# Optimization experiments

Measured on AMD Instinct MI355X. Metric: run time of the kernel, lower is better.

Reference implementation:

```python
import jax, jax.numpy as jnp
from jax import lax
import numpy as np

VOCAB, EMB, SEQ, HID, BATCH = 50000, 300, 80, 128, 4096


def setup_inputs() -> dict:
    key = jax.random.key(0)
    ks = jax.random.split(key, 7)
    x = jax.random.randint(ks[0], (BATCH, SEQ), 0, VOCAB)
    emb = jax.random.normal(ks[1], (VOCAB, EMB), jnp.float32) * 0.05  # frozen pretrained table
    # Keras SimpleRNN: kernel (glorot), recurrent_kernel (orthogonal-ish), bias zeros
    Wxh = jax.random.normal(ks[2], (EMB, HID), jnp.float32) * (1.0 / np.sqrt(EMB))
    Whh = jax.random.normal(ks[3], (HID, HID), jnp.float32) * (1.0 / np.sqrt(HID))
    bh = jnp.zeros((HID,), jnp.float32)
    Wd = jax.random.normal(ks[4], (HID, 1), jnp.float32) * (1.0 / np.sqrt(HID))
    bd = jnp.zeros((1,), jnp.float32)
    return {"x": x, "emb": emb, "Wxh": Wxh, "Whh": Whh, "bh": bh, "Wd": Wd, "bd": bd}


def reference(x, emb, Wxh, Whh, bh, Wd, bd):
    # Embedding lookup: [B, T] -> [B, T, E]
    e = emb[x]
    # Precompute input projection for all timesteps: [B, T, H]
    xp = jnp.einsum('bte,eh->bth', e, Wxh) + bh
    # SimpleRNN recurrence (tanh), return only last hidden state
    def step(h, xt):  # xt: [B, H]
        h = jnp.tanh(xt + h @ Whh)
        return h, None
    h0 = jnp.zeros((x.shape[0], Whh.shape[0]), xp.dtype)
    h_last, _ = lax.scan(step, h0, jnp.swapaxes(xp, 0, 1))  # scan over time
    # Dense(1, sigmoid): [B, 1]
    return jax.nn.sigmoid(h_last @ Wd + bd)
```

## Files before the change

kernel.cpp:

```cpp
#include <hip/hip_runtime.h>
#include <hip/hip_fp16.h>
#include <cstdint>

#define VOCAB 50000
#define EMB   300
#define SEQ   80
#define HID   128
#define BATCH 4096

typedef __attribute__((ext_vector_type(8))) _Float16 f16x8;
typedef __attribute__((ext_vector_type(4))) float    f32x4;

static __device__ __forceinline__ float fast_tanh(float xv) {
    const float e = __expf(2.f * xv);
    float r;
    asm("v_rcp_f32 %0, %1" : "=v"(r) : "v"(e + 1.f));
    return fmaf(-2.f, r, 1.f);
}
static __device__ __forceinline__ float f16b2f(unsigned short u) {
    _Float16 h; __builtin_memcpy(&h, &u, 2); return (float)h;
}
static __device__ __forceinline__ unsigned pack2h(float a, float b) {
    _Float16 ha = (_Float16)a, hb = (_Float16)b;
    unsigned short ua, ub;
    __builtin_memcpy(&ua, &ha, 2); __builtin_memcpy(&ub, &hb, 2);
    return (unsigned)ua | ((unsigned)ub << 16);
}

__global__ __launch_bounds__(256) void k_wprep(const float* __restrict__ Wxh,
                                               _Float16* __restrict__ W2) {
    const int c = blockIdx.x * 256 + threadIdx.x;
    if (c >= 5120) return;
    const int ks = c >> 9, rem = c & 511, col = rem >> 2, g = rem & 3;
    f16x8 f;
    #pragma unroll
    for (int j = 0; j < 8; ++j) {
        const int k = 32 * ks + 8 * g + j;
        f[j] = (_Float16)(k < EMB ? Wxh[k * HID + col] : 0.f);
    }
    *reinterpret_cast<f16x8*>(W2 + (size_t)c * 8) = f;
}

__global__ __launch_bounds__(256, 2) void k_ptab(
    const float*    __restrict__ emb,
    const _Float16* __restrict__ W2,
    const float*    __restrict__ bh,
    float*          __restrict__ P)
{
    const int tid = threadIdx.x, lane = tid & 63;
    const int wv = tid >> 6, r16 = lane & 15, g = lane >> 4;
    const int row = blockIdx.x * 64 + wv * 16 + r16;
    const float* rp = emb + (size_t)(row < VOCAB ? row : VOCAB - 1) * EMB;
    const bool wr = (row < VOCAB);

    f16x8 ef[10];
    #pragma unroll
    for (int ks = 0; ks < 9; ++ks) {
        const float4 u0 = *reinterpret_cast<const float4*>(rp + 32 * ks + 8 * g);
        const float4 u1 = *reinterpret_cast<const float4*>(rp + 32 * ks + 8 * g + 4);
        f16x8 f;
        f[0] = (_Float16)u0.x; f[1] = (_Float16)u0.y;
        f[2] = (_Float16)u0.z; f[3] = (_Float16)u0.w;
        f[4] = (_Float16)u1.x; f[5] = (_Float16)u1.y;
        f[6] = (_Float16)u1.z; f[7] = (_Float16)u1.w;
        ef[ks] = f;
    }
    {
        f16x8 f;
        #pragma unroll
        for (int j = 0; j < 8; ++j) f[j] = (_Float16)0.f;
        if (g == 0) {
            const float4 u0 = *reinterpret_cast<const float4*>(rp + 288);
            const float4 u1 = *reinterpret_cast<const float4*>(rp + 292);
            f[0] = (_Float16)u0.x; f[1] = (_Float16)u0.y;
            f[2] = (_Float16)u0.z; f[3] = (_Float16)u0.w;
            f[4] = (_Float16)u1.x; f[5] = (_Float16)u1.y;
            f[6] = (_Float16)u1.z; f[7] = (_Float16)u1.w;
        } else if (g == 1) {
            const float4 u0 = *reinterpret_cast<const float4*>(rp + 296);
            f[0] = (_Float16)u0.x; f[1] = (_Float16)u0.y;
            f[2] = (_Float16)u0.z; f[3] = (_Float16)u0.w;
        }
        ef[9] = f;
    }

    float4 bhf[8];
    #pragma unroll
    for (int ct = 0; ct < 8; ++ct)
        bhf[ct] = *reinterpret_cast<const float4*>(bh + 16 * ct + 4 * g);

    f16x8 wA[10], wB[10];
    #pragma unroll
    for (int ks = 0; ks < 10; ++ks)
        wA[ks] = *reinterpret_cast<const f16x8*>(
            W2 + ((size_t)ks * 512 + (size_t)r16 * 4 + g) * 8);

    float* const po = P + (size_t)(wr ? row : 0) * HID;

    #pragma unroll
    for (int ct = 0; ct < 8; ++ct) {
        if (ct < 7) {
            const int coln = 16 * (ct + 1) + r16;
            #pragma unroll
            for (int ks = 0; ks < 10; ++ks)
                ((ct & 1) ? wA : wB)[ks] = *reinterpret_cast<const f16x8*>(
                    W2 + ((size_t)ks * 512 + (size_t)coln * 4 + g) * 8);
        }
        const f16x8* wc = (ct & 1) ? wB : wA;
        f32x4 a0 = {0.f, 0.f, 0.f, 0.f}, a1 = {0.f, 0.f, 0.f, 0.f};
        #pragma unroll
        for (int ks = 0; ks < 10; ks += 2) {
            a0 = __builtin_amdgcn_mfma_f32_16x16x32_f16(wc[ks],     ef[ks],     a0, 0, 0, 0);
            a1 = __builtin_amdgcn_mfma_f32_16x16x32_f16(wc[ks + 1], ef[ks + 1], a1, 0, 0, 0);
        }
        float4 o;
        o.x = a0[0] + a1[0] + bhf[ct].x;
        o.y = a0[1] + a1[1] + bhf[ct].y;
        o.z = a0[2] + a1[2] + bhf[ct].z;
        o.w = a0[3] + a1[3] + bhf[ct].w;
        if (wr) *reinterpret_cast<float4*>(po + ct * 16 + g * 4) = o;
    }
}

__global__ __launch_bounds__(512, 2) void k_rnn(
    const int*   __restrict__ x,
    const float* __restrict__ P,
    const float* __restrict__ Whh,
    const float* __restrict__ Wd,
    const float* __restrict__ bd,
    float*       __restrict__ out)
{
    __shared__ __align__(16) unsigned char Hb[2][16 * 256];

    const int tid = threadIdx.x, lane = tid & 63, wv = tid >> 6;
    const int r16 = lane & 15, g = lane >> 4;
    const int rb = blockIdx.x * 16;
    const int xbase = (rb + r16) * SEQ;

    if (tid < 256) { uint4 z = {}; *reinterpret_cast<uint4*>(&Hb[0][tid * 16]) = z; }

    const int col = 16 * wv + r16;

    int h_rd[4];
    #pragma unroll
    for (int ks = 0; ks < 4; ++ks)
        h_rd[ks] = r16 * 256 + (((4 * ks + g) ^ r16) & 15) * 16;
    const int hw = r16 * 256 + (((2 * wv + (g >> 1)) ^ r16) & 15) * 16 + (g & 1) * 8;

    f16x8 wh[4];
    #pragma unroll
    for (int ks = 0; ks < 4; ++ks) {
        f16x8 f;
        #pragma unroll
        for (int j = 0; j < 8; ++j)
            f[j] = (_Float16)Whh[(32 * ks + 8 * g + j) * HID + col];
        wh[ks] = f;
    }

    const int goff = 16 * wv + 4 * g;
    f32x4 xgA, xgB;
    int idxA, idxB;
    {
        const int i0 = x[xbase + 0];
        const int i1 = x[xbase + 1];
        xgA = *reinterpret_cast<const f32x4*>(P + (size_t)i0 * HID + goff);
        xgB = *reinterpret_cast<const f32x4*>(P + (size_t)i1 * HID + goff);
        idxA = x[xbase + 2];
        idxB = x[xbase + 3];
    }

    __syncthreads();

    const f32x4 z4 = {0.f, 0.f, 0.f, 0.f};
    f32x4 accA, accB;

#define STEP(T, PB, XG, IDX)                                                       \
    {                                                                              \
        const unsigned char* hb = &Hb[PB][0];                                      \
        const f16x8 h0 = *reinterpret_cast<const f16x8*>(hb + h_rd[0]);            \
        const f16x8 h1 = *reinterpret_cast<const f16x8*>(hb + h_rd[1]);            \
        const f16x8 h2 = *reinterpret_cast<const f16x8*>(hb + h_rd[2]);            \
        const f16x8 h3 = *reinterpret_cast<const f16x8*>(hb + h_rd[3]);            \
        accA = __builtin_amdgcn_mfma_f32_16x16x32_f16(wh[0], h0, XG, 0, 0, 0);     \
        accB = __builtin_amdgcn_mfma_f32_16x16x32_f16(wh[1], h1, z4, 0, 0, 0);     \
        accA = __builtin_amdgcn_mfma_f32_16x16x32_f16(wh[2], h2, accA, 0, 0, 0);   \
        accB = __builtin_amdgcn_mfma_f32_16x16x32_f16(wh[3], h3, accB, 0, 0, 0);   \
                  \
        if ((T) + 2 < SEQ) {                                                       \
            XG = *reinterpret_cast<const f32x4*>(P + (size_t)(IDX) * HID + goff);  \
            if ((T) + 4 < SEQ) IDX = x[xbase + (T) + 4];                           \
        }                                                                          \
        uint2 hv;                                                                  \
        hv.x = pack2h(fast_tanh(accA[0] + accB[0]), fast_tanh(accA[1] + accB[1])); \
        hv.y = pack2h(fast_tanh(accA[2] + accB[2]), fast_tanh(accA[3] + accB[3])); \
        *reinterpret_cast<uint2*>(&Hb[(PB) ^ 1][hw]) = hv;                         \
        asm volatile("s_waitcnt lgkmcnt(0)" ::: "memory");                         \
        __builtin_amdgcn_s_barrier();                                              \
        __builtin_amdgcn_sched_barrier(0);                                         \
    }

    #pragma unroll 1
    for (int t = 0; t < SEQ; t += 2) {
        STEP(t,     0, xgA, idxA);
        STEP(t + 1, 1, xgB, idxB);
    }
#undef STEP

    const char* hb0 = (const char*)&Hb[0][0];
    const int r = tid >> 5, m = tid & 31;
    const int fb = r * 256 + (((m >> 1) ^ r) & 15) * 16 + (m & 1) * 8;
    const uint2 hv = *reinterpret_cast<const uint2*>(hb0 + fb);
    const float4 wd = *reinterpret_cast<const float4*>(&Wd[4 * m]);
    float part = f16b2f((unsigned short)(hv.x & 0xffff)) * wd.x
               + f16b2f((unsigned short)(hv.x >> 16))    * wd.y
               + f16b2f((unsigned short)(hv.y & 0xffff)) * wd.z
               + f16b2f((unsigned short)(hv.y >> 16))    * wd.w;
    part += __shfl_down(part, 16, 32);
    part += __shfl_down(part, 8, 32);
    part += __shfl_down(part, 4, 32);
    part += __shfl_down(part, 2, 32);
    part += __shfl_down(part, 1, 32);
    if (m == 0) out[rb + r] = 1.f / (1.f + expf(-(part + bd[0])));
}

extern "C" void kernel_launch(void* const* d_in, const int* in_sizes, int n_in,
                              void* d_out, int out_size, void* d_ws, size_t ws_size,
                              hipStream_t stream)
{
    (void)in_sizes; (void)n_in; (void)out_size; (void)ws_size;
    const int*   x   = (const int*)  d_in[0];
    const float* emb = (const float*)d_in[1];
    const float* Wxh = (const float*)d_in[2];
    const float* Whh = (const float*)d_in[3];
    const float* bh  = (const float*)d_in[4];
    const float* Wd  = (const float*)d_in[5];
    const float* bd  = (const float*)d_in[6];
    float* out = (float*)d_out;

    float*    P  = (float*)d_ws;
    _Float16* W2 = (_Float16*)((char*)d_ws + 25600000);

    k_wprep<<<20, 256, 0, stream>>>(Wxh, W2);
    k_ptab<<<(VOCAB + 63) / 64, 256, 0, stream>>>(emb, W2, bh, P);
    k_rnn<<<BATCH / 16, 512, 0, stream>>>(x, P, Whh, Wd, bd, out);
}
```

Before: 81.65 us.

## Store projection table in fp16 and stage per-step gathers through LDS

The precomputed vocab projection table P is now written in fp16, which halves its size and the write/read traffic in both kernels. In the RNN kernel the token indices for the block are preloaded into LDS. Half the threads gather full 256-byte P rows as coalesced 16-byte loads into a double-buffered LDS tile one step ahead, and each wave reads its slice from LDS as the MFMA accumulator init. This costs extra LDS traffic per step and a small fp16 rounding of the input projection, and the step loop is no longer held to unroll 1.

```diff
diff --git a/kernel.cpp b/kernel.cpp
--- a/kernel.cpp
+++ b/kernel.cpp
@@ -45,7 +45,7 @@
     const float*    __restrict__ emb,
     const _Float16* __restrict__ W2,
     const float*    __restrict__ bh,
-    float*          __restrict__ P)
+    _Float16*       __restrict__ P)
 {
     const int tid = threadIdx.x, lane = tid & 63;
     const int wv = tid >> 6, r16 = lane & 15, g = lane >> 4;
@@ -95,7 +95,7 @@
         wA[ks] = *reinterpret_cast<const f16x8*>(
             W2 + ((size_t)ks * 512 + (size_t)r16 * 4 + g) * 8);
 
-    float* const po = P + (size_t)(wr ? row : 0) * HID;
+    unsigned short* const po = (unsigned short*)P + (size_t)(wr ? row : 0) * HID;
 
     #pragma unroll
     for (int ct = 0; ct < 8; ++ct) {
@@ -113,30 +113,30 @@
             a0 = __builtin_amdgcn_mfma_f32_16x16x32_f16(wc[ks],     ef[ks],     a0, 0, 0, 0);
             a1 = __builtin_amdgcn_mfma_f32_16x16x32_f16(wc[ks + 1], ef[ks + 1], a1, 0, 0, 0);
         }
-        float4 o;
-        o.x = a0[0] + a1[0] + bhf[ct].x;
-        o.y = a0[1] + a1[1] + bhf[ct].y;
-        o.z = a0[2] + a1[2] + bhf[ct].z;
-        o.w = a0[3] + a1[3] + bhf[ct].w;
-        if (wr) *reinterpret_cast<float4*>(po + ct * 16 + g * 4) = o;
+        uint2 o;
+        o.x = pack2h(a0[0] + a1[0] + bhf[ct].x, a0[1] + a1[1] + bhf[ct].y);
+        o.y = pack2h(a0[2] + a1[2] + bhf[ct].z, a0[3] + a1[3] + bhf[ct].w);
+        if (wr) *reinterpret_cast<uint2*>(po + ct * 16 + g * 4) = o;
     }
 }
 
 __global__ __launch_bounds__(512, 2) void k_rnn(
-    const int*   __restrict__ x,
-    const float* __restrict__ P,
-    const float* __restrict__ Whh,
-    const float* __restrict__ Wd,
-    const float* __restrict__ bd,
-    float*       __restrict__ out)
+    const int*      __restrict__ x,
+    const _Float16* __restrict__ P,
+    const float*    __restrict__ Whh,
+    const float*    __restrict__ Wd,
+    const float*    __restrict__ bd,
+    float*          __restrict__ out)
 {
+    __shared__ __align__(16) unsigned char Xb[2][16 * 256];
     __shared__ __align__(16) unsigned char Hb[2][16 * 256];
+    __shared__ int xidx[16 * SEQ];
 
     const int tid = threadIdx.x, lane = tid & 63, wv = tid >> 6;
     const int r16 = lane & 15, g = lane >> 4;
     const int rb = blockIdx.x * 16;
-    const int xbase = (rb + r16) * SEQ;
-
+
+    for (int q = tid; q < 16 * SEQ; q += 512) xidx[q] = x[rb * SEQ + q];
     if (tid < 256) { uint4 z = {}; *reinterpret_cast<uint4*>(&Hb[0][tid * 16]) = z; }
 
     const int col = 16 * wv + r16;
@@ -157,39 +157,44 @@
         wh[ks] = f;
     }
 
-    const int goff = 16 * wv + 4 * g;
-    f32x4 xgA, xgB;
-    int idxA, idxB;
-    {
-        const int i0 = x[xbase + 0];
-        const int i1 = x[xbase + 1];
-        xgA = *reinterpret_cast<const f32x4*>(P + (size_t)i0 * HID + goff);
-        xgB = *reinterpret_cast<const f32x4*>(P + (size_t)i1 * HID + goff);
-        idxA = x[xbase + 2];
-        idxB = x[xbase + 3];
-    }
+    const bool gon  = (tid < 256);
+    const int  grow = (tid >> 4) & 15, gk = tid & 15;
+    const int  gdst = grow * 256 + ((gk ^ grow) & 15) * 16;
 
     __syncthreads();
 
-    const f32x4 z4 = {0.f, 0.f, 0.f, 0.f};
-    f32x4 accA, accB;
-
-#define STEP(T, PB, XG, IDX)                                                       \
+    if (gon)
+        *reinterpret_cast<uint4*>(&Xb[0][gdst]) = *reinterpret_cast<const uint4*>(
+            P + (size_t)xidx[grow * SEQ] * HID + 8 * gk);
+    uint4 cur = {}, nxt = {};
+    if (gon) cur = *reinterpret_cast<const uint4*>(
+        P + (size_t)xidx[grow * SEQ + 1] * HID + 8 * gk);
+
+    asm volatile("s_waitcnt lgkmcnt(0)" ::: "memory");
+    __builtin_amdgcn_s_barrier();
+    __builtin_amdgcn_sched_barrier(0);
+
+#define STEP(T, PB, CUR, NXT)                                                      \
     {                                                                              \
-        const unsigned char* hb = &Hb[PB][0];                                      \
-        const f16x8 h0 = *reinterpret_cast<const f16x8*>(hb + h_rd[0]);            \
-        const f16x8 h1 = *reinterpret_cast<const f16x8*>(hb + h_rd[1]);            \
-        const f16x8 h2 = *reinterpret_cast<const f16x8*>(hb + h_rd[2]);            \
-        const f16x8 h3 = *reinterpret_cast<const f16x8*>(hb + h_rd[3]);            \
-        accA = __builtin_amdgcn_mfma_f32_16x16x32_f16(wh[0], h0, XG, 0, 0, 0);     \
-        accB = __builtin_amdgcn_mfma_f32_16x16x32_f16(wh[1], h1, z4, 0, 0, 0);     \
+        if ((T) + 1 < SEQ && gon)                                                  \
+            *reinterpret_cast<uint4*>(&Xb[(PB) ^ 1][gdst]) = CUR;                  \
+        if ((T) + 2 < SEQ && gon)                                                  \
+            NXT = *reinterpret_cast<const uint4*>(                                 \
+                P + (size_t)xidx[grow * SEQ + (T) + 2] * HID + 8 * gk);            \
+        const uint2 xv = *reinterpret_cast<const uint2*>(&Xb[PB][hw]);             \
+        f32x4 accA, accB = {0.f, 0.f, 0.f, 0.f};                                   \
+        accA[0] = f16b2f((unsigned short)(xv.x & 0xffff));                         \
+        accA[1] = f16b2f((unsigned short)(xv.x >> 16));                            \
+        accA[2] = f16b2f((unsigned short)(xv.y & 0xffff));                         \
+        accA[3] = f16b2f((unsigned short)(xv.y >> 16));                            \
+        const f16x8 h0 = *reinterpret_cast<const f16x8*>(&Hb[PB][h_rd[0]]);        \
+        const f16x8 h1 = *reinterpret_cast<const f16x8*>(&Hb[PB][h_rd[1]]);        \
+        const f16x8 h2 = *reinterpret_cast<const f16x8*>(&Hb[PB][h_rd[2]]);        \
+        const f16x8 h3 = *reinterpret_cast<const f16x8*>(&Hb[PB][h_rd[3]]);        \
+        accA = __builtin_amdgcn_mfma_f32_16x16x32_f16(wh[0], h0, accA, 0, 0, 0);   \
+        accB = __builtin_amdgcn_mfma_f32_16x16x32_f16(wh[1], h1, accB, 0, 0, 0);   \
         accA = __builtin_amdgcn_mfma_f32_16x16x32_f16(wh[2], h2, accA, 0, 0, 0);   \
         accB = __builtin_amdgcn_mfma_f32_16x16x32_f16(wh[3], h3, accB, 0, 0, 0);   \
-                  \
-        if ((T) + 2 < SEQ) {                                                       \
-            XG = *reinterpret_cast<const f32x4*>(P + (size_t)(IDX) * HID + goff);  \
-            if ((T) + 4 < SEQ) IDX = x[xbase + (T) + 4];                           \
-        }                                                                          \
         uint2 hv;                                                                  \
         hv.x = pack2h(fast_tanh(accA[0] + accB[0]), fast_tanh(accA[1] + accB[1])); \
         hv.y = pack2h(fast_tanh(accA[2] + accB[2]), fast_tanh(accA[3] + accB[3])); \
@@ -199,10 +204,9 @@
         __builtin_amdgcn_sched_barrier(0);                                         \
     }
 
-    #pragma unroll 1
     for (int t = 0; t < SEQ; t += 2) {
-        STEP(t,     0, xgA, idxA);
-        STEP(t + 1, 1, xgB, idxB);
+        STEP(t,     0, cur, nxt);
+        STEP(t + 1, 1, nxt, cur);
     }
 #undef STEP
 
@@ -237,8 +241,8 @@
     const float* bd  = (const float*)d_in[6];
     float* out = (float*)d_out;
 
-    float*    P  = (float*)d_ws;
-    _Float16* W2 = (_Float16*)((char*)d_ws + 25600000);
+    _Float16* P  = (_Float16*)d_ws;
+    _Float16* W2 = (_Float16*)((char*)d_ws + 12800000);
 
     k_wprep<<<20, 256, 0, stream>>>(Wxh, W2);
     k_ptab<<<(VOCAB + 63) / 64, 256, 0, stream>>>(emb, W2, bh, P);
```

Result: faster. 73.11 us (-10.5%).
